# Optimization experiments

Measured on AMD Instinct MI355X. Metric: run time of the kernel, lower is better.

## Reference

```python
import jax, jax.numpy as jnp
import numpy as np

H, E, K = 1024, 8, 2  # hidden_size, num_experts, top_k
B, S = 2, 4096


def setup_inputs() -> dict:
    key = jax.random.key(0)
    ks = jax.random.split(key, 5)
    s = 1.0 / np.sqrt(H)
    return {
        "x": jax.random.normal(ks[0], (B, S, H), dtype=jnp.float32),
        "ln_scale": jnp.ones((H,), jnp.float32),
        "ln_bias": jnp.zeros((H,), jnp.float32),
        "w1": (jax.random.normal(ks[1], (H, H), jnp.float32) * s),
        "b1": jnp.zeros((H,), jnp.float32),
        "w2": (jax.random.normal(ks[2], (H, E), jnp.float32) * s),
        "b2": jnp.zeros((E,), jnp.float32),
        "We": (jax.random.normal(ks[3], (E, H, H), jnp.float32) * s),
        "be": jnp.zeros((E, H), jnp.float32),
    }


def _layernorm(x, scale, bias, eps=1e-5):
    m = jnp.mean(x, axis=-1, keepdims=True)
    v = jnp.var(x, axis=-1, keepdims=True)
    return (x - m) * jax.lax.rsqrt(v + eps) * scale + bias


def reference(x, ln_scale, ln_bias, w1, b1, w2, b2, We, be):
    b, s, h = x.shape
    # --- router (BaseRouter): LN -> MLP -> softmax -> top-k -> renorm ---
    xn = _layernorm(x, ln_scale, ln_bias)
    hmid = jax.nn.relu(xn @ w1 + b1)
    logits = hmid @ w2 + b2                      # [B,S,E]
    probs = jax.nn.softmax(logits, axis=-1)
    topk_p, topk_i = jax.lax.top_k(probs, K)     # [B,S,K]
    topk_p = topk_p / jnp.sum(topk_p, axis=-1, keepdims=True)
    # sparse combine weights [B,S,E]: renormalized top-k gate, 0 elsewhere
    cw = jnp.sum(topk_p[..., None] * jax.nn.one_hot(topk_i, E, dtype=x.dtype), axis=-2)
    # --- expert dispatch / weighted combine ---
    t = b * s
    xf = x.reshape(t, h)
    cwf = cw.reshape(t, E)
    ye = jnp.einsum('th,ehd->etd', xf, We) + be[:, None, :]   # [E,T,H]
    out = jnp.einsum('te,etd->td', cwf, ye).reshape(b, s, h)
    # --- aux load-balance loss ---
    mean_p = jnp.mean(probs, axis=(0, 1))        # [E]
    aux = jnp.sum(mean_p * jnp.log(mean_p * E + 1e-9))
    return out, aux
```

## Files before the change

kernel.cpp:

```cpp
#include <hip/hip_runtime.h>
#include <hip/hip_fp16.h>

#define H 1024
#define E 8
#define TT 8192

typedef __attribute__((ext_vector_type(8))) short bf16x8;
typedef __attribute__((ext_vector_type(4))) float f32x4;

__device__ __forceinline__ unsigned short f2bf(float f) {
  unsigned int u = __float_as_uint(f);
  u += 0x7fffu + ((u >> 16) & 1u);
  return (unsigned short)(u >> 16);
}

__device__ __forceinline__ int swz(int row, int c) {
  return (row << 5) | (((c ^ (row >> 1)) & 3) << 3);
}

__global__ __launch_bounds__(64) void k_init(int* cnt, double* psum) {
  int t = threadIdx.x;
  if (t < E) { cnt[t] = 0; psum[t] = 0.0; }
}

__global__ __launch_bounds__(256) void k_cast_we(const float* __restrict__ we, unsigned short* __restrict__ wet) {
  __shared__ unsigned short tile[32][33];
  int e = blockIdx.z;
  int kb = blockIdx.x << 5, nb = blockIdx.y << 5;
  int t = threadIdx.x;
  int cc = t & 31, rr = t >> 5;
  size_t base = (size_t)e * H * H;
#pragma unroll
  for (int r = 0; r < 4; ++r) {
    int k = kb + rr + (r << 3);
    tile[rr + (r << 3)][cc] = f2bf(we[base + (size_t)k * H + nb + cc]);
  }
  __syncthreads();
#pragma unroll
  for (int r = 0; r < 4; ++r) {
    int n = nb + rr + (r << 3);
    wet[base + (size_t)n * H + kb + cc] = tile[cc][rr + (r << 3)];
  }
}

__global__ __launch_bounds__(256) void k_cast_w1(const float* __restrict__ w1, const float* __restrict__ lsc,
                                                 unsigned short* __restrict__ w1h, unsigned short* __restrict__ w1l) {
  __shared__ float tile[32][33];
  int kb = blockIdx.x << 5, nb = blockIdx.y << 5;
  int t = threadIdx.x;
  int cc = t & 31, rr = t >> 5;
#pragma unroll
  for (int r = 0; r < 4; ++r) {
    int k = kb + rr + (r << 3);
    tile[rr + (r << 3)][cc] = w1[(size_t)k * H + nb + cc] * lsc[k];
  }
  __syncthreads();
#pragma unroll
  for (int r = 0; r < 4; ++r) {
    int n = nb + rr + (r << 3);
    float v = tile[cc][rr + (r << 3)];
    unsigned short h = f2bf(v);
    float hv = __uint_as_float((unsigned)h << 16);
    unsigned short l = f2bf(v - hv);
    w1h[(size_t)n * H + kb + cc] = h;
    w1l[(size_t)n * H + kb + cc] = l;
  }
}

__global__ __launch_bounds__(256) void k_b1a(const float* __restrict__ w1, const float* __restrict__ lbi,
                                             float* __restrict__ part) {
  int bk = blockIdx.x, t = threadIdx.x;
  float a0 = 0, a1 = 0, a2 = 0, a3 = 0;
  for (int kk = 0; kk < 16; ++kk) {
    int k = (bk << 4) + kk;
    float lb = lbi[k];
    const float* row = &w1[(size_t)k * H];
    a0 = fmaf(lb, row[t], a0);
    a1 = fmaf(lb, row[t + 256], a1);
    a2 = fmaf(lb, row[t + 512], a2);
    a3 = fmaf(lb, row[t + 768], a3);
  }
  part[bk * H + t] = a0;
  part[bk * H + t + 256] = a1;
  part[bk * H + t + 512] = a2;
  part[bk * H + t + 768] = a3;
}

__global__ __launch_bounds__(256) void k_b1b(const float* __restrict__ part, const float* __restrict__ b1,
                                             float* __restrict__ b1eff) {
  int n = (blockIdx.x << 8) + threadIdx.x;
  float s = b1[n];
  for (int j = 0; j < 64; ++j) s += part[j * H + n];
  b1eff[n] = s;
}

__global__ __launch_bounds__(256) void k_stats(const float* __restrict__ x, float2* __restrict__ stats,
                                               unsigned short* __restrict__ xb) {
  int tok = blockIdx.x, t = threadIdx.x;
  const float4 v = *reinterpret_cast<const float4*>(&x[(size_t)tok * H + (t << 2)]);
  float s = v.x + v.y + v.z + v.w;
  float ss = v.x * v.x + v.y * v.y + v.z * v.z + v.w * v.w;
#pragma unroll
  for (int off = 32; off; off >>= 1) { s += __shfl_down(s, off); ss += __shfl_down(ss, off); }
  __shared__ float red[4][2];
  int lane = t & 63, wv = t >> 6;
  if (lane == 0) { red[wv][0] = s; red[wv][1] = ss; }
  __syncthreads();
  float fs = red[0][0] + red[1][0] + red[2][0] + red[3][0];
  float fss = red[0][1] + red[1][1] + red[2][1] + red[3][1];
  float mean = fs * (1.0f / H);
  float var = fss * (1.0f / H) - mean * mean;
  float rstd = rsqrtf(var + 1e-5f);
  if (t == 0) stats[tok] = make_float2(mean, rstd);
  ushort4 ob;
  ob.x = f2bf(v.x); ob.y = f2bf(v.y); ob.z = f2bf(v.z); ob.w = f2bf(v.w);
  *reinterpret_cast<ushort4*>(&xb[(size_t)tok * H + (t << 2)]) = ob;
}

__global__ __launch_bounds__(256) void k_router_mfma(
    const float* __restrict__ x, const float2* __restrict__ stats,
    const unsigned short* __restrict__ w1h, const unsigned short* __restrict__ w1l,
    const float* __restrict__ b1eff, const float* __restrict__ w2, float* __restrict__ plog) {
  __shared__ __align__(16) short Ah[4096], Al[4096], Bh[4096], Bl[4096];
  __shared__ float2 st[128];
  int t = threadIdx.x;
  int bm = blockIdx.x << 7, bn = blockIdx.y << 7;
  if (t < 128) st[t] = stats[bm + t];
  __syncthreads();
  int arow = t >> 1, ac0 = (t & 1) << 1;
  int brow = t >> 2, bc = t & 3;
  float2 mr = st[arow];
  float rs = mr.y, mb = -mr.x * mr.y;
  const float* xsrc = &x[(size_t)(bm + arow) * H + (ac0 << 3)];
  const unsigned short* s1 = &w1h[(size_t)(bn + brow) * H + (bc << 3)];
  const unsigned short* s2 = &w1h[(size_t)(bn + brow + 64) * H + (bc << 3)];
  const unsigned short* s3 = &w1l[(size_t)(bn + brow) * H + (bc << 3)];
  const unsigned short* s4 = &w1l[(size_t)(bn + brow + 64) * H + (bc << 3)];
  float4 va0 = *(const float4*)(xsrc + 0), va1 = *(const float4*)(xsrc + 4);
  float4 va2 = *(const float4*)(xsrc + 8), va3 = *(const float4*)(xsrc + 12);
  int4 vb0 = *(const int4*)s1, vb1 = *(const int4*)s2, vb2 = *(const int4*)s3, vb3 = *(const int4*)s4;
  int lane = t & 63, wv = t >> 6;
  int wr = (wv >> 1) << 6, wc = (wv & 1) << 6;
  int l15 = lane & 15, lgp = lane >> 4;
  f32x4 acc[4][4];
#pragma unroll
  for (int i = 0; i < 4; ++i)
#pragma unroll
    for (int j = 0; j < 4; ++j) acc[i][j] = f32x4{0.f, 0.f, 0.f, 0.f};
  for (int kt = 0; kt < 32; ++kt) {
    float zz[16];
    zz[0] = fmaf(va0.x, rs, mb); zz[1] = fmaf(va0.y, rs, mb);
    zz[2] = fmaf(va0.z, rs, mb); zz[3] = fmaf(va0.w, rs, mb);
    zz[4] = fmaf(va1.x, rs, mb); zz[5] = fmaf(va1.y, rs, mb);
    zz[6] = fmaf(va1.z, rs, mb); zz[7] = fmaf(va1.w, rs, mb);
    zz[8] = fmaf(va2.x, rs, mb); zz[9] = fmaf(va2.y, rs, mb);
    zz[10] = fmaf(va2.z, rs, mb); zz[11] = fmaf(va2.w, rs, mb);
    zz[12] = fmaf(va3.x, rs, mb); zz[13] = fmaf(va3.y, rs, mb);
    zz[14] = fmaf(va3.z, rs, mb); zz[15] = fmaf(va3.w, rs, mb);
    unsigned hw[8], lw[8];
#pragma unroll
    for (int p = 0; p < 8; ++p) {
      unsigned ua = __float_as_uint(zz[2 * p]), ub = __float_as_uint(zz[2 * p + 1]);
      hw[p] = (ua >> 16) | (ub & 0xffff0000u);
      float la = zz[2 * p] - __uint_as_float(ua & 0xffff0000u);
      float lb = zz[2 * p + 1] - __uint_as_float(ub & 0xffff0000u);
      lw[p] = (__float_as_uint(la) >> 16) | (__float_as_uint(lb) & 0xffff0000u);
    }
    __syncthreads();
    *(int4*)&Ah[swz(arow, ac0)] = make_int4(hw[0], hw[1], hw[2], hw[3]);
    *(int4*)&Ah[swz(arow, ac0 + 1)] = make_int4(hw[4], hw[5], hw[6], hw[7]);
    *(int4*)&Al[swz(arow, ac0)] = make_int4(lw[0], lw[1], lw[2], lw[3]);
    *(int4*)&Al[swz(arow, ac0 + 1)] = make_int4(lw[4], lw[5], lw[6], lw[7]);
    *(int4*)&Bh[swz(brow, bc)] = vb0;
    *(int4*)&Bh[swz(brow + 64, bc)] = vb1;
    *(int4*)&Bl[swz(brow, bc)] = vb2;
    *(int4*)&Bl[swz(brow + 64, bc)] = vb3;
    __syncthreads();
    if (kt + 1 < 32) {
      xsrc += 32; s1 += 32; s2 += 32; s3 += 32; s4 += 32;
      va0 = *(const float4*)(xsrc + 0); va1 = *(const float4*)(xsrc + 4);
      va2 = *(const float4*)(xsrc + 8); va3 = *(const float4*)(xsrc + 12);
      vb0 = *(const int4*)s1; vb1 = *(const int4*)s2; vb2 = *(const int4*)s3; vb3 = *(const int4*)s4;
    }
    bf16x8 bh[4], bl[4];
#pragma unroll
    for (int j = 0; j < 4; ++j) {
      bh[j] = *(const bf16x8*)&Bh[swz(wc + (j << 4) + l15, lgp)];
      bl[j] = *(const bf16x8*)&Bl[swz(wc + (j << 4) + l15, lgp)];
    }
#pragma unroll
    for (int i = 0; i < 4; ++i) {
      bf16x8 ah = *(const bf16x8*)&Ah[swz(wr + (i << 4) + l15, lgp)];
      bf16x8 al = *(const bf16x8*)&Al[swz(wr + (i << 4) + l15, lgp)];
#pragma unroll
      for (int j = 0; j < 4; ++j) {
        acc[i][j] = __builtin_amdgcn_mfma_f32_16x16x32_bf16(ah, bh[j], acc[i][j], 0, 0, 0);
        acc[i][j] = __builtin_amdgcn_mfma_f32_16x16x32_bf16(ah, bl[j], acc[i][j], 0, 0, 0);
        acc[i][j] = __builtin_amdgcn_mfma_f32_16x16x32_bf16(al, bh[j], acc[i][j], 0, 0, 0);
      }
    }
  }
  float w2r[4][8], b1r[4];
#pragma unroll
  for (int j = 0; j < 4; ++j) {
    int col = bn + wc + (j << 4) + l15;
    float4 p0 = *(const float4*)&w2[(size_t)col * E];
    float4 p1 = *(const float4*)&w2[(size_t)col * E + 4];
    w2r[j][0] = p0.x; w2r[j][1] = p0.y; w2r[j][2] = p0.z; w2r[j][3] = p0.w;
    w2r[j][4] = p1.x; w2r[j][5] = p1.y; w2r[j][6] = p1.z; w2r[j][7] = p1.w;
    b1r[j] = b1eff[col];
  }
#pragma unroll
  for (int i = 0; i < 4; ++i)
#pragma unroll
    for (int j = 0; j < 4; ++j)
#pragma unroll
      for (int r = 0; r < 4; ++r) acc[i][j][r] = fmaxf(acc[i][j][r] + b1r[j], 0.f);
  int wh = wc >> 6;
  size_t pbase = ((size_t)(blockIdx.y * 2 + wh) * TT + bm) * E;
#pragma unroll
  for (int e = 0; e < E; ++e) {
    float se[4][4];
#pragma unroll
    for (int i = 0; i < 4; ++i)
#pragma unroll
      for (int r = 0; r < 4; ++r)
        se[i][r] = acc[i][0][r] * w2r[0][e] + acc[i][1][r] * w2r[1][e] +
                   acc[i][2][r] * w2r[2][e] + acc[i][3][r] * w2r[3][e];
#pragma unroll
    for (int off = 1; off < 16; off <<= 1)
#pragma unroll
      for (int i = 0; i < 4; ++i)
#pragma unroll
        for (int r = 0; r < 4; ++r) se[i][r] += __shfl_xor(se[i][r], off);
    if (l15 == 0) {
#pragma unroll
      for (int i = 0; i < 4; ++i)
#pragma unroll
        for (int r = 0; r < 4; ++r) {
          int row = wr + (i << 4) + (lgp << 2) + r;
          plog[pbase + (size_t)row * E + e] = se[i][r];
        }
    }
  }
}

__global__ __launch_bounds__(256) void k_top(const float* __restrict__ plog, const float* __restrict__ b2,
                                             int* __restrict__ topE, float* __restrict__ topW,
                                             int* __restrict__ listIdx, float* __restrict__ listW,
                                             int* __restrict__ cnt, double* __restrict__ psum) {
  int t = threadIdx.x, lane = t & 63;
  int tok = (blockIdx.x << 8) + t;
  float lg[E], p[E];
  float4 ba = *reinterpret_cast<const float4*>(b2);
  float4 bb = *reinterpret_cast<const float4*>(b2 + 4);
  lg[0] = ba.x; lg[1] = ba.y; lg[2] = ba.z; lg[3] = ba.w;
  lg[4] = bb.x; lg[5] = bb.y; lg[6] = bb.z; lg[7] = bb.w;
#pragma unroll
  for (int nb = 0; nb < 16; ++nb) {
    const float* pp = &plog[((size_t)nb * TT + tok) * E];
    float4 q0 = *reinterpret_cast<const float4*>(pp);
    float4 q1 = *reinterpret_cast<const float4*>(pp + 4);
    lg[0] += q0.x; lg[1] += q0.y; lg[2] += q0.z; lg[3] += q0.w;
    lg[4] += q1.x; lg[5] += q1.y; lg[6] += q1.z; lg[7] += q1.w;
  }
  float m = lg[0];
#pragma unroll
  for (int e = 1; e < E; ++e) m = fmaxf(m, lg[e]);
  float s = 0.f;
#pragma unroll
  for (int e = 0; e < E; ++e) { p[e] = __expf(lg[e] - m); s += p[e]; }
  float inv = 1.f / s;
#pragma unroll
  for (int e = 0; e < E; ++e) p[e] *= inv;
  {
    float ps[E];
#pragma unroll
    for (int e = 0; e < E; ++e) ps[e] = p[e];
#pragma unroll
    for (int off = 1; off < 64; off <<= 1)
#pragma unroll
      for (int e = 0; e < E; ++e) ps[e] += __shfl_xor(ps[e], off);
    if (lane == 0)
#pragma unroll
      for (int e = 0; e < E; ++e) atomicAdd(&psum[e], (double)ps[e]);
  }
  int e0 = 0;
#pragma unroll
  for (int e = 1; e < E; ++e) if (p[e] > p[e0]) e0 = e;
  int e1 = (e0 == 0) ? 1 : 0;
#pragma unroll
  for (int e = 0; e < E; ++e) if (e != e0 && p[e] > p[e1]) e1 = e;
  float rsw = 1.f / (p[e0] + p[e1]);
  float w0 = p[e0] * rsw, w1v = p[e1] * rsw;
  topE[tok << 1] = e0; topE[(tok << 1) + 1] = e1;
  topW[tok << 1] = w0; topW[(tok << 1) + 1] = w1v;
  unsigned long long lt = (1ull << lane) - 1ull;
#pragma unroll
  for (int e = 0; e < E; ++e) {
    unsigned long long m0 = __ballot(e0 == e);
    unsigned long long m1 = __ballot(e1 == e);
    int n0 = __popcll(m0), total = n0 + __popcll(m1);
    if (total == 0) continue;
    int leader = __ffsll(m0 | m1) - 1;
    int base = 0;
    if (lane == leader) base = atomicAdd(&cnt[e], total);
    base = __shfl(base, leader);
    if (e0 == e) {
      int pos = e * TT + base + __popcll(m0 & lt);
      listIdx[pos] = (tok << 1); listW[pos] = w0;
    }
    if (e1 == e) {
      int pos = e * TT + base + n0 + __popcll(m1 & lt);
      listIdx[pos] = (tok << 1) | 1; listW[pos] = w1v;
    }
  }
}

__global__ __launch_bounds__(256) void k_expert_gemm(const unsigned short* __restrict__ xb,
                                                     const unsigned short* __restrict__ wet,
                                                     const int* __restrict__ listIdx, const float* __restrict__ listW,
                                                     const int* __restrict__ cnt, unsigned short* __restrict__ ys) {
  int e = blockIdx.z;
  int c = cnt[e];
  int r0 = blockIdx.x << 7;
  if (r0 >= c) return;
  int n0 = blockIdx.y << 7;
  __shared__ __align__(16) short A[4096], B[4096];
  __shared__ int gi[128];
  __shared__ float gw[128];
  int t = threadIdx.x;
  if (t < 128) {
    int rr = r0 + t;
    gi[t] = (rr < c) ? listIdx[e * TT + rr] : -1;
    gw[t] = (rr < c) ? listW[e * TT + rr] : 0.f;
  }
  __syncthreads();
  int brow = t >> 2, bc = t & 3;
  int pk1 = gi[brow], pk2 = gi[brow + 64];
  int tokA1 = (pk1 < 0) ? 0 : (pk1 >> 1);
  int tokA2 = (pk2 < 0) ? 0 : (pk2 >> 1);
  const unsigned short* a1 = &xb[(size_t)tokA1 * H + (bc << 3)];
  const unsigned short* a2 = &xb[(size_t)tokA2 * H + (bc << 3)];
  size_t wbase = (size_t)e * H * H;
  const unsigned short* b1 = &wet[wbase + (size_t)(n0 + brow) * H + (bc << 3)];
  const unsigned short* b2 = &wet[wbase + (size_t)(n0 + brow + 64) * H + (bc << 3)];
  int4 va0 = *(const int4*)a1, va1 = *(const int4*)a2;
  int4 vb0 = *(const int4*)b1, vb1 = *(const int4*)b2;
  int lane = t & 63, wv = t >> 6;
  int wr = (wv >> 1) << 6, wc = (wv & 1) << 6;
  int l15 = lane & 15, lgp = lane >> 4;
  f32x4 acc[4][4];
#pragma unroll
  for (int i = 0; i < 4; ++i)
#pragma unroll
    for (int j = 0; j < 4; ++j) acc[i][j] = f32x4{0.f, 0.f, 0.f, 0.f};
  for (int kt = 0; kt < 32; ++kt) {
    __syncthreads();
    *(int4*)&A[swz(brow, bc)] = va0;
    *(int4*)&A[swz(brow + 64, bc)] = va1;
    *(int4*)&B[swz(brow, bc)] = vb0;
    *(int4*)&B[swz(brow + 64, bc)] = vb1;
    __syncthreads();
    if (kt + 1 < 32) {
      a1 += 32; a2 += 32; b1 += 32; b2 += 32;
      va0 = *(const int4*)a1; va1 = *(const int4*)a2;
      vb0 = *(const int4*)b1; vb1 = *(const int4*)b2;
    }
    bf16x8 bq[4];
#pragma unroll
    for (int j = 0; j < 4; ++j) bq[j] = *(const bf16x8*)&B[swz(wc + (j << 4) + l15, lgp)];
#pragma unroll
    for (int i = 0; i < 4; ++i) {
      bf16x8 af = *(const bf16x8*)&A[swz(wr + (i << 4) + l15, lgp)];
#pragma unroll
      for (int j = 0; j < 4; ++j)
        acc[i][j] = __builtin_amdgcn_mfma_f32_16x16x32_bf16(af, bq[j], acc[i][j], 0, 0, 0);
    }
  }
#pragma unroll
  for (int i = 0; i < 4; ++i) {
#pragma unroll
    for (int r = 0; r < 4; ++r) {
      int row = wr + (i << 4) + (lgp << 2) + r;
      int pk = gi[row];
      if (pk < 0) continue;
      int tok = pk >> 1, slot = pk & 1;
      float w = gw[row];
      size_t ob = ((size_t)slot * TT + tok) * H + n0 + wc + l15;
#pragma unroll
      for (int j = 0; j < 4; ++j) ys[ob + (j << 4)] = __half_as_ushort(__float2half(w * acc[i][j][r]));
    }
  }
}

__global__ __launch_bounds__(256) void k_combine(const unsigned short* __restrict__ ys, const int* __restrict__ topE,
                                                 const float* __restrict__ topW, const float* __restrict__ be,
                                                 float* __restrict__ out) {
  int tok = blockIdx.x, t = threadIdx.x;
  int e0 = topE[tok << 1], e1 = topE[(tok << 1) + 1];
  float w0 = topW[tok << 1], w1v = topW[(tok << 1) + 1];
  int h = t << 2;
  size_t base = (size_t)tok * H + h;
  ushort4 a = *reinterpret_cast<const ushort4*>(&ys[base]);
  ushort4 b = *reinterpret_cast<const ushort4*>(&ys[(size_t)TT * H + base]);
  float4 b0 = *reinterpret_cast<const float4*>(&be[e0 * H + h]);
  float4 b1v = *reinterpret_cast<const float4*>(&be[e1 * H + h]);
  float4 o;
  o.x = __half2float(__ushort_as_half(a.x)) + __half2float(__ushort_as_half(b.x)) + w0 * b0.x + w1v * b1v.x;
  o.y = __half2float(__ushort_as_half(a.y)) + __half2float(__ushort_as_half(b.y)) + w0 * b0.y + w1v * b1v.y;
  o.z = __half2float(__ushort_as_half(a.z)) + __half2float(__ushort_as_half(b.z)) + w0 * b0.z + w1v * b1v.z;
  o.w = __half2float(__ushort_as_half(a.w)) + __half2float(__ushort_as_half(b.w)) + w0 * b0.w + w1v * b1v.w;
  *reinterpret_cast<float4*>(&out[base]) = o;
}

__global__ __launch_bounds__(64) void k_aux(const double* __restrict__ psum, float* __restrict__ outAux) {
  if (threadIdx.x == 0) {
    double a = 0.0;
    for (int e = 0; e < E; ++e) {
      double mp = psum[e] / (double)TT;
      a += mp * log(mp * (double)E + 1e-9);
    }
    outAux[0] = (float)a;
  }
}

extern "C" void kernel_launch(void* const* d_in, const int* in_sizes, int n_in, void* d_out, int out_size, void* d_ws,
                              size_t ws_size, hipStream_t stream) {
  const float* x = (const float*)d_in[0];
  const float* lsc = (const float*)d_in[1];
  const float* lbi = (const float*)d_in[2];
  const float* w1 = (const float*)d_in[3];
  const float* b1 = (const float*)d_in[4];
  const float* w2 = (const float*)d_in[5];
  const float* b2 = (const float*)d_in[6];
  const float* we = (const float*)d_in[7];
  const float* be = (const float*)d_in[8];
  float* out = (float*)d_out;
  char* ws = (char*)d_ws;

  char* p = ws;
  float2* stats = (float2*)p; p += TT * 8;
  int* topE = (int*)p; p += TT * 2 * 4;
  float* topW = (float*)p; p += TT * 2 * 4;
  int* listIdx = (int*)p; p += E * TT * 4;
  float* listW = (float*)p; p += E * TT * 4;
  int* cnt = (int*)p; p += 256;
  double* psum = (double*)p; p += 2048;
  float* b1eff = (float*)p; p += H * 4;
  float* part = (float*)p; p += 64 * H * 4;
  unsigned short* xb = (unsigned short*)(ws + (2u << 20));
  unsigned short* wet = (unsigned short*)(ws + (18u << 20));
  unsigned short* w1h = (unsigned short*)(ws + (34u << 20));
  unsigned short* w1l = (unsigned short*)(ws + (36u << 20));
  float* plog = (float*)(ws + (38u << 20));
  unsigned short* ys = (unsigned short*)(ws + (34u << 20));

  k_init<<<1, 64, 0, stream>>>(cnt, psum);
  k_cast_w1<<<dim3(32, 32), 256, 0, stream>>>(w1, lsc, w1h, w1l);
  k_b1a<<<64, 256, 0, stream>>>(w1, lbi, part);
  k_b1b<<<4, 256, 0, stream>>>(part, b1, b1eff);
  k_cast_we<<<dim3(32, 32, E), 256, 0, stream>>>(we, wet);
  k_stats<<<TT, 256, 0, stream>>>(x, stats, xb);
  k_router_mfma<<<dim3(TT / 128, H / 128), 256, 0, stream>>>(x, stats, w1h, w1l, b1eff, w2, plog);
  k_top<<<TT / 256, 256, 0, stream>>>(plog, b2, topE, topW, listIdx, listW, cnt, psum);
  k_expert_gemm<<<dim3(TT / 128, H / 128, E), 256, 0, stream>>>(xb, wet, listIdx, listW, cnt, ys);
  k_combine<<<TT, 256, 0, stream>>>(ys, topE, topW, be, out);
  k_aux<<<1, 64, 0, stream>>>(psum, out + (size_t)TT * H);
}
```

Before: 227.5 us.

## Double-buffer expert GEMM with direct LDS loads, compact work list, fuse setup kernels

The expert GEMM now loads its tiles straight into LDS with global_load_lds, double-buffered, using explicit waitcnt, barriers and a raised priority around the MFMA block. A new scheduling kernel builds a compact work list that interleaves blocks across experts, so the grid no longer launches many empty blocks. The bias pre-reduction moves into the w1 cast kernel and the counter init into k_b1b, which removes two launches. The expert weight cast is moved later in the stream. The trade-off is more LDS per block and an extra tiny single-block launch.

```diff
diff --git a/kernel.cpp b/kernel.cpp
--- a/kernel.cpp
+++ b/kernel.cpp
@@ -18,9 +18,9 @@
   return (row << 5) | (((c ^ (row >> 1)) & 3) << 3);
 }
 
-__global__ __launch_bounds__(64) void k_init(int* cnt, double* psum) {
-  int t = threadIdx.x;
-  if (t < E) { cnt[t] = 0; psum[t] = 0.0; }
+__device__ __forceinline__ void gld16(void* lds, const void* g) {
+  __builtin_amdgcn_global_load_lds((const __attribute__((address_space(1))) void*)g,
+                                   (__attribute__((address_space(3))) void*)lds, 16, 0, 0);
 }
 
 __global__ __launch_bounds__(256) void k_cast_we(const float* __restrict__ we, unsigned short* __restrict__ wet) {
@@ -44,21 +44,38 @@
 }
 
 __global__ __launch_bounds__(256) void k_cast_w1(const float* __restrict__ w1, const float* __restrict__ lsc,
-                                                 unsigned short* __restrict__ w1h, unsigned short* __restrict__ w1l) {
+                                                 const float* __restrict__ lbi, unsigned short* __restrict__ w1h,
+                                                 unsigned short* __restrict__ w1l, float* __restrict__ part) {
   __shared__ float tile[32][33];
+  __shared__ float red[8][33];
   int kb = blockIdx.x << 5, nb = blockIdx.y << 5;
   int t = threadIdx.x;
   int cc = t & 31, rr = t >> 5;
 #pragma unroll
   for (int r = 0; r < 4; ++r) {
     int k = kb + rr + (r << 3);
-    tile[rr + (r << 3)][cc] = w1[(size_t)k * H + nb + cc] * lsc[k];
-  }
-  __syncthreads();
+    tile[rr + (r << 3)][cc] = w1[(size_t)k * H + nb + cc];
+  }
+  __syncthreads();
+  float pp = 0.f;
+#pragma unroll
+  for (int r = 0; r < 4; ++r) {
+    int kk = rr + (r << 3);
+    pp = fmaf(lbi[kb + kk], tile[kk][cc], pp);
+  }
+  red[rr][cc] = pp;
+  float scale = lsc[kb + cc];
+  __syncthreads();
+  if (rr == 0) {
+    float s = 0.f;
+#pragma unroll
+    for (int j = 0; j < 8; ++j) s += red[j][cc];
+    part[blockIdx.x * H + nb + cc] = s;
+  }
 #pragma unroll
   for (int r = 0; r < 4; ++r) {
     int n = nb + rr + (r << 3);
-    float v = tile[cc][rr + (r << 3)];
+    float v = tile[cc][rr + (r << 3)] * scale;
     unsigned short h = f2bf(v);
     float hv = __uint_as_float((unsigned)h << 16);
     unsigned short l = f2bf(v - hv);
@@ -67,31 +84,15 @@
   }
 }
 
-__global__ __launch_bounds__(256) void k_b1a(const float* __restrict__ w1, const float* __restrict__ lbi,
-                                             float* __restrict__ part) {
-  int bk = blockIdx.x, t = threadIdx.x;
-  float a0 = 0, a1 = 0, a2 = 0, a3 = 0;
-  for (int kk = 0; kk < 16; ++kk) {
-    int k = (bk << 4) + kk;
-    float lb = lbi[k];
-    const float* row = &w1[(size_t)k * H];
-    a0 = fmaf(lb, row[t], a0);
-    a1 = fmaf(lb, row[t + 256], a1);
-    a2 = fmaf(lb, row[t + 512], a2);
-    a3 = fmaf(lb, row[t + 768], a3);
-  }
-  part[bk * H + t] = a0;
-  part[bk * H + t + 256] = a1;
-  part[bk * H + t + 512] = a2;
-  part[bk * H + t + 768] = a3;
-}
-
 __global__ __launch_bounds__(256) void k_b1b(const float* __restrict__ part, const float* __restrict__ b1,
-                                             float* __restrict__ b1eff) {
-  int n = (blockIdx.x << 8) + threadIdx.x;
+                                             float* __restrict__ b1eff, int* __restrict__ cnt,
+                                             double* __restrict__ psum) {
+  int t = threadIdx.x;
+  int n = (blockIdx.x << 8) + t;
   float s = b1[n];
-  for (int j = 0; j < 64; ++j) s += part[j * H + n];
+  for (int j = 0; j < 32; ++j) s += part[j * H + n];
   b1eff[n] = s;
+  if (blockIdx.x == 0 && t < E) { cnt[t] = 0; psum[t] = 0.0; }
 }
 
 __global__ __launch_bounds__(256) void k_stats(const float* __restrict__ x, float2* __restrict__ stats,
@@ -317,16 +318,38 @@
   }
 }
 
+#define WL_SLOTS 2560
+__global__ __launch_bounds__(256) void k_sched(const int* __restrict__ cnt, int* __restrict__ workList) {
+  int t = threadIdx.x;
+  for (int i = t; i < WL_SLOTS; i += 256) workList[i] = -1;
+  __syncthreads();
+  if (t < E) {
+    int e = t;
+    int nb = (cnt[e] + 127) >> 7;
+    int ov = 2048 + (e << 6);
+    int g = 0;
+    for (int bx = 0; bx < nb; ++bx) {
+      for (int by = 0; by < 8; ++by) {
+        int item = (e << 12) | (bx << 4) | by;
+        int slot = (g < 256) ? ((g << 3) + e) : ov++;
+        workList[slot] = item;
+        ++g;
+      }
+    }
+  }
+}
+
 __global__ __launch_bounds__(256) void k_expert_gemm(const unsigned short* __restrict__ xb,
                                                      const unsigned short* __restrict__ wet,
                                                      const int* __restrict__ listIdx, const float* __restrict__ listW,
-                                                     const int* __restrict__ cnt, unsigned short* __restrict__ ys) {
-  int e = blockIdx.z;
+                                                     const int* __restrict__ cnt, const int* __restrict__ workList,
+                                                     unsigned short* __restrict__ ys) {
+  int item = workList[blockIdx.x];
+  if (item < 0) return;
+  int e = item >> 12, bx = (item >> 4) & 255, by = item & 15;
   int c = cnt[e];
-  int r0 = blockIdx.x << 7;
-  if (r0 >= c) return;
-  int n0 = blockIdx.y << 7;
-  __shared__ __align__(16) short A[4096], B[4096];
+  int r0 = bx << 7, n0 = by << 7;
+  __shared__ __align__(16) short A[2][4096], Bs[2][4096];
   __shared__ int gi[128];
   __shared__ float gw[128];
   int t = threadIdx.x;
@@ -336,46 +359,56 @@
     gw[t] = (rr < c) ? listW[e * TT + rr] : 0.f;
   }
   __syncthreads();
-  int brow = t >> 2, bc = t & 3;
-  int pk1 = gi[brow], pk2 = gi[brow + 64];
-  int tokA1 = (pk1 < 0) ? 0 : (pk1 >> 1);
-  int tokA2 = (pk2 < 0) ? 0 : (pk2 >> 1);
-  const unsigned short* a1 = &xb[(size_t)tokA1 * H + (bc << 3)];
-  const unsigned short* a2 = &xb[(size_t)tokA2 * H + (bc << 3)];
+  int w = t >> 6, lane = t & 63;
+  int l15 = lane & 15, lgp = lane >> 4;
+  int wr = (w >> 1) << 6, wc = (w & 1) << 6;
+  int s0 = (w << 7) + lane, s1 = s0 + 64;
+  int rA0 = s0 >> 2, cg0 = (s0 & 3) ^ ((rA0 >> 1) & 3);
+  int rA1 = s1 >> 2, cg1 = (s1 & 3) ^ ((rA1 >> 1) & 3);
+  int pk0 = gi[rA0], pk1 = gi[rA1];
+  const unsigned short* srcA0 = xb + (size_t)((pk0 < 0) ? 0 : (pk0 >> 1)) * H + (cg0 << 3);
+  const unsigned short* srcA1 = xb + (size_t)((pk1 < 0) ? 0 : (pk1 >> 1)) * H + (cg1 << 3);
   size_t wbase = (size_t)e * H * H;
-  const unsigned short* b1 = &wet[wbase + (size_t)(n0 + brow) * H + (bc << 3)];
-  const unsigned short* b2 = &wet[wbase + (size_t)(n0 + brow + 64) * H + (bc << 3)];
-  int4 va0 = *(const int4*)a1, va1 = *(const int4*)a2;
-  int4 vb0 = *(const int4*)b1, vb1 = *(const int4*)b2;
-  int lane = t & 63, wv = t >> 6;
-  int wr = (wv >> 1) << 6, wc = (wv & 1) << 6;
-  int l15 = lane & 15, lgp = lane >> 4;
+  const unsigned short* srcB0 = wet + wbase + (size_t)(n0 + rA0) * H + (cg0 << 3);
+  const unsigned short* srcB1 = wet + wbase + (size_t)(n0 + rA1) * H + (cg1 << 3);
+  int d0 = (w << 10), d1 = d0 + 512;
   f32x4 acc[4][4];
 #pragma unroll
   for (int i = 0; i < 4; ++i)
 #pragma unroll
     for (int j = 0; j < 4; ++j) acc[i][j] = f32x4{0.f, 0.f, 0.f, 0.f};
+  gld16(&A[0][d0], srcA0); gld16(&A[0][d1], srcA1);
+  gld16(&Bs[0][d0], srcB0); gld16(&Bs[0][d1], srcB1);
+#pragma unroll
   for (int kt = 0; kt < 32; ++kt) {
-    __syncthreads();
-    *(int4*)&A[swz(brow, bc)] = va0;
-    *(int4*)&A[swz(brow + 64, bc)] = va1;
-    *(int4*)&B[swz(brow, bc)] = vb0;
-    *(int4*)&B[swz(brow + 64, bc)] = vb1;
-    __syncthreads();
-    if (kt + 1 < 32) {
-      a1 += 32; a2 += 32; b1 += 32; b2 += 32;
-      va0 = *(const int4*)a1; va1 = *(const int4*)a2;
-      vb0 = *(const int4*)b1; vb1 = *(const int4*)b2;
-    }
+    const int cur = kt & 1, nxt = cur ^ 1;
+    if (kt < 31) {
+      const int ko = (kt + 1) << 5;
+      gld16(&A[nxt][d0], srcA0 + ko); gld16(&A[nxt][d1], srcA1 + ko);
+      gld16(&Bs[nxt][d0], srcB0 + ko); gld16(&Bs[nxt][d1], srcB1 + ko);
+      asm volatile("s_waitcnt vmcnt(4)" ::: "memory");
+    } else {
+      asm volatile("s_waitcnt vmcnt(0)" ::: "memory");
+    }
+    __builtin_amdgcn_sched_barrier(0);
+    __builtin_amdgcn_s_barrier();
+    __builtin_amdgcn_sched_barrier(0);
     bf16x8 bq[4];
 #pragma unroll
-    for (int j = 0; j < 4; ++j) bq[j] = *(const bf16x8*)&B[swz(wc + (j << 4) + l15, lgp)];
-#pragma unroll
-    for (int i = 0; i < 4; ++i) {
-      bf16x8 af = *(const bf16x8*)&A[swz(wr + (i << 4) + l15, lgp)];
+    for (int j = 0; j < 4; ++j) bq[j] = *(const bf16x8*)&Bs[cur][swz(wc + (j << 4) + l15, lgp)];
+    bf16x8 aq[4];
+#pragma unroll
+    for (int i = 0; i < 4; ++i) aq[i] = *(const bf16x8*)&A[cur][swz(wr + (i << 4) + l15, lgp)];
+    __builtin_amdgcn_s_setprio(1);
+#pragma unroll
+    for (int i = 0; i < 4; ++i)
 #pragma unroll
       for (int j = 0; j < 4; ++j)
-        acc[i][j] = __builtin_amdgcn_mfma_f32_16x16x32_bf16(af, bq[j], acc[i][j], 0, 0, 0);
+        acc[i][j] = __builtin_amdgcn_mfma_f32_16x16x32_bf16(aq[i], bq[j], acc[i][j], 0, 0, 0);
+    __builtin_amdgcn_s_setprio(0);
+    if (kt < 31) {
+      __builtin_amdgcn_sched_barrier(0);
+      __builtin_amdgcn_s_barrier();
     }
   }
 #pragma unroll
@@ -386,10 +419,10 @@
       int pk = gi[row];
       if (pk < 0) continue;
       int tok = pk >> 1, slot = pk & 1;
-      float w = gw[row];
+      float wgt = gw[row];
       size_t ob = ((size_t)slot * TT + tok) * H + n0 + wc + l15;
 #pragma unroll
-      for (int j = 0; j < 4; ++j) ys[ob + (j << 4)] = __half_as_ushort(__float2half(w * acc[i][j][r]));
+      for (int j = 0; j < 4; ++j) ys[ob + (j << 4)] = __half_as_ushort(__float2half(wgt * acc[i][j][r]));
     }
   }
 }
@@ -440,7 +473,6 @@
   char* ws = (char*)d_ws;
 
   char* p = ws;
-  float2* stats = (float2*)p; p += TT * 8;
   int* topE = (int*)p; p += TT * 2 * 4;
   float* topW = (float*)p; p += TT * 2 * 4;
   int* listIdx = (int*)p; p += E * TT * 4;
@@ -448,23 +480,24 @@
   int* cnt = (int*)p; p += 256;
   double* psum = (double*)p; p += 2048;
   float* b1eff = (float*)p; p += H * 4;
-  float* part = (float*)p; p += 64 * H * 4;
-  unsigned short* xb = (unsigned short*)(ws + (2u << 20));
-  unsigned short* wet = (unsigned short*)(ws + (18u << 20));
-  unsigned short* w1h = (unsigned short*)(ws + (34u << 20));
-  unsigned short* w1l = (unsigned short*)(ws + (36u << 20));
-  float* plog = (float*)(ws + (38u << 20));
-  unsigned short* ys = (unsigned short*)(ws + (34u << 20));
-
-  k_init<<<1, 64, 0, stream>>>(cnt, psum);
-  k_cast_w1<<<dim3(32, 32), 256, 0, stream>>>(w1, lsc, w1h, w1l);
-  k_b1a<<<64, 256, 0, stream>>>(w1, lbi, part);
-  k_b1b<<<4, 256, 0, stream>>>(part, b1, b1eff);
-  k_cast_we<<<dim3(32, 32, E), 256, 0, stream>>>(we, wet);
+  float* part = (float*)p; p += 32 * H * 4;
+  int* workList = (int*)p; p += WL_SLOTS * 4;
+  float2* stats = (float2*)p; p += TT * 8;
+  unsigned short* xb = (unsigned short*)(ws + (2ull << 20));
+  unsigned short* wet = (unsigned short*)(ws + (18ull << 20));
+  unsigned short* w1h = (unsigned short*)(ws + (34ull << 20));
+  unsigned short* w1l = (unsigned short*)(ws + (36ull << 20));
+  float* plog = (float*)(ws + (38ull << 20));
+  unsigned short* ys = (unsigned short*)(ws + (34ull << 20));
+
+  k_cast_w1<<<dim3(32, 32), 256, 0, stream>>>(w1, lsc, lbi, w1h, w1l, part);
+  k_b1b<<<4, 256, 0, stream>>>(part, b1, b1eff, cnt, psum);
   k_stats<<<TT, 256, 0, stream>>>(x, stats, xb);
   k_router_mfma<<<dim3(TT / 128, H / 128), 256, 0, stream>>>(x, stats, w1h, w1l, b1eff, w2, plog);
   k_top<<<TT / 256, 256, 0, stream>>>(plog, b2, topE, topW, listIdx, listW, cnt, psum);
-  k_expert_gemm<<<dim3(TT / 128, H / 128, E), 256, 0, stream>>>(xb, wet, listIdx, listW, cnt, ys);
+  k_sched<<<1, 256, 0, stream>>>(cnt, workList);
+  k_cast_we<<<dim3(32, 32, E), 256, 0, stream>>>(we, wet);
+  k_expert_gemm<<<WL_SLOTS, 256, 0, stream>>>(xb, wet, listIdx, listW, cnt, workList, ys);
   k_combine<<<TT, 256, 0, stream>>>(ys, topE, topW, be, out);
   k_aux<<<1, 64, 0, stream>>>(psum, out + (size_t)TT * H);
 }
```

Result: faster. 220.0 us (-3.3%).
